# Kernel optimization log

Hardware: AMD Instinct MI355X
Metric: run time of the kernel (lower is better)

The kernel has to match this reference:

```python
import jax, jax.numpy as jnp
import numpy as np

B, K, N, D, E, EE, H, P = 512, 64, 1024, 128, 100000, 1024, 256, 12

def setup_inputs() -> dict:
    key = jax.random.key(0)
    ks = jax.random.split(key, 6)
    return {
        'ts_emb': jax.random.normal(ks[0], (B, D, N), jnp.float32),
        'event_table': jax.random.normal(ks[1], (E, EE), jnp.float32),
        'W_t': jax.random.normal(ks[2], (H, EE), jnp.float32) * 0.02,
        'b_t': jnp.zeros((H,), jnp.float32),
        'W_mm': jax.random.normal(ks[3], (P, H + D), jnp.float32) * 0.02,
        'b_mm': jnp.zeros((P,), jnp.float32),
        'W_ts': jax.random.normal(ks[4], (P, D), jnp.float32) * 0.02,
        'b_ts': jnp.zeros((P,), jnp.float32),
        'event_idx': jax.random.randint(ks[5], (B, K), 0, E, jnp.int64) if jax.config.read('jax_enable_x64') else jax.random.randint(ks[5], (B, K), 0, E, jnp.int32),
        'event_mask': jnp.ones((B, K), bool),
    }

def reference(ts_emb, event_table, W_t, b_t, W_mm, b_mm, W_ts, b_ts, event_idx, event_mask):
    h = W_t.shape[0]  # hidden_event_emb_dim
    # ragged event gather: [B, K, EE]
    ev = event_table[event_idx]
    # Linear(EE -> H): [B, K, H]
    ev_h = jnp.einsum('bke,he->bkh', ev, W_t) + b_t
    # masked max over events (event_fuse_type='max'): [B, H]
    neg = jnp.asarray(-jnp.inf, ev_h.dtype)
    ev_emb = jnp.max(jnp.where(event_mask[:, :, None], ev_h, neg), axis=1)
    # mm_forecaster = Conv1d(H+D -> P, k=1) on cat([event_emb repeat N, ts_emb]);
    # split the channel-wise linear so the broadcast part is never materialized.
    mm_ev = ev_emb @ W_mm[:, :h].T                       # [B, P]
    mm_ts = jnp.einsum('pd,bdn->bpn', W_mm[:, h:], ts_emb)  # [B, P, N]
    mm_pred = mm_ev[:, :, None] + mm_ts + b_mm[None, :, None]
    # ts_forecaster = Conv1d(D -> P, k=1)
    ts_pred = jnp.einsum('pd,bdn->bpn', W_ts, ts_emb) + b_ts[None, :, None]
    return (ts_pred + mm_pred) * 0.5
```

## Files before the change

### kernel.cpp

```cpp
#include <hip/hip_runtime.h>
#include <hip/hip_bf16.h>
#include <math.h>

#define B_   512
#define KEV  64
#define NN   1024
#define DD   128
#define EE_  1024
#define HH   256
#define PP   12
#define BKE  256
#define NSE  (EE_ / BKE)

typedef __bf16 bf16x8 __attribute__((ext_vector_type(8)));
typedef float  f32x4  __attribute__((ext_vector_type(4)));

static __device__ __forceinline__ unsigned short f2bf(float f) {
    unsigned int u = __builtin_bit_cast(unsigned int, f);
    u = (u + 0x7FFFu + ((u >> 16) & 1u)) >> 16;
    return (unsigned short)u;
}

__global__ __launch_bounds__(256) void prep_kernel(
    const float* __restrict__ Wt,
    const float* __restrict__ Wmm,
    const float* __restrict__ Wts,
    const unsigned int* __restrict__ idxW,
    const unsigned int* __restrict__ mskW,
    unsigned short* __restrict__ WtBf,
    float* __restrict__ Wc,
    int* __restrict__ flags)
{
    if (blockIdx.x < 256) {
        int i4 = (blockIdx.x * 256 + threadIdx.x) * 4;
        const float4 v = *reinterpret_cast<const float4*>(Wt + i4);
        ushort4 o = make_ushort4(f2bf(v.x), f2bf(v.y), f2bf(v.z), f2bf(v.w));
        *reinterpret_cast<ushort4*>(WtBf + i4) = o;
        return;
    }
    __shared__ int any_nz;
    if (threadIdx.x == 0) any_nz = 0;
    __syncthreads();
    int local = 0;
    for (int k = threadIdx.x; k < (B_ * KEV) / 2; k += 256)
        local |= (idxW[2 * k + 1] != 0u);
    if (local) atomicOr(&any_nz, 1);
    for (int k = threadIdx.x; k < PP * DD; k += 256) {
        int p = k >> 7, d = k & 127;
        Wc[k] = Wmm[p * (HH + DD) + HH + d] + Wts[p * DD + d];
    }
    __syncthreads();
    if (threadIdx.x == 0) {
        flags[0] = any_nz ? 0 : 1;
        unsigned int w0 = mskW[0], w1 = mskW[1];
        flags[1] = (w0 == 0x01010101u) ? 0 : ((w1 == 0u) ? 2 : 1);
    }
}

__global__ __launch_bounds__(256, 2) void event_kernel(
    const float* __restrict__ table,
    const void* __restrict__ idxRaw,
    const void* __restrict__ maskRaw,
    const int* __restrict__ flags,
    const unsigned short* __restrict__ WtBf,
    const float* __restrict__ bt,
    const float* __restrict__ Wmm,
    const float* __restrict__ bmm,
    const float* __restrict__ bts,
    float* __restrict__ cOut)
{
    const int b = blockIdx.x;
    const int t = threadIdx.x;
    const int w = t >> 6;
    const int l = t & 63;

    __shared__ __align__(16) unsigned short sA[2][64 * BKE];
    __shared__ int           sIdx[KEV];
    __shared__ unsigned char sMask[KEV];
    __shared__ float         sEv[HH];

    if (t < KEV) {
        const int i = b * KEV + t;
        int id;
        if (flags[0]) id = (int)((const long long*)idxRaw)[i];
        else          id = ((const int*)idxRaw)[i];
        sIdx[t] = id;
        const int mm = flags[1];
        bool mk;
        if      (mm == 0) mk = ((const unsigned char*)maskRaw)[i] != 0;
        else if (mm == 1) mk = ((const int*)maskRaw)[i] != 0;
        else              mk = ((const long long*)maskRaw)[i] != 0;
        sMask[t] = mk ? 1 : 0;
    }
    __syncthreads();

    const float* ptr[16];
    #pragma unroll
    for (int i = 0; i < 16; ++i)
        ptr[i] = table + (size_t)sIdx[w * 16 + i] * EE_ + (l << 2);

    auto loadstep = [&](int s, f32x4 (&r)[16]) {
        #pragma unroll
        for (int i = 0; i < 16; ++i)
            r[i] = *reinterpret_cast<const f32x4*>(ptr[i] + s * BKE);
    };
    auto writebuf = [&](int bufi, const f32x4 (&r)[16]) {
        #pragma unroll
        for (int i = 0; i < 16; ++i) {
            const int row = w * 16 + i;
            const int sw  = ((row & 7) << 3) ^ ((row & 8) << 1);
            ushort4 o = make_ushort4(f2bf(r[i][0]), f2bf(r[i][1]),
                                     f2bf(r[i][2]), f2bf(r[i][3]));
            *reinterpret_cast<ushort4*>(
                &sA[bufi][row * BKE + (((l << 2)) ^ sw)]) = o;
        }
    };

    const int lm = l & 15;
    const int lg = l >> 4;

    f32x4 acc[4][4];
    #pragma unroll
    for (int mi = 0; mi < 4; ++mi)
        #pragma unroll
        for (int ni = 0; ni < 4; ++ni)
            acc[mi][ni] = (f32x4){0.f, 0.f, 0.f, 0.f};

    const unsigned short* wtB = WtBf + (size_t)(w * 64 + lm) * EE_ + lg * 8;

    auto mfma_step = [&](int cur, int s) {
        #pragma unroll
        for (int ks = 0; ks < 8; ++ks) {
            bf16x8 af[4];
            #pragma unroll
            for (int mi = 0; mi < 4; ++mi) {
                const int row = mi * 16 + lm;
                const int e   = ks * 32 + lg * 8;
                const int es  = e ^ (((row & 7) << 3) ^ ((row & 8) << 1));
                af[mi] = *reinterpret_cast<const bf16x8*>(&sA[cur][row * BKE + es]);
            }
            #pragma unroll
            for (int ni = 0; ni < 4; ++ni) {
                const unsigned short* bp = wtB + (size_t)ni * 16 * EE_ + s * BKE + ks * 32;
                bf16x8 bfr = *reinterpret_cast<const bf16x8*>(bp);
                #pragma unroll
                for (int mi = 0; mi < 4; ++mi)
                    acc[mi][ni] = __builtin_amdgcn_mfma_f32_16x16x32_bf16(
                        af[mi], bfr, acc[mi][ni], 0, 0, 0);
            }
        }
    };

    f32x4 rA[16];
    loadstep(0, rA);
    writebuf(0, rA);
    __syncthreads();

    #pragma unroll 1
    for (int s = 0; s < NSE; ++s) {
        if (s + 1 < NSE) loadstep(s + 1, rA);
        mfma_step(s & 1, s);
        if (s + 1 < NSE) writebuf((s + 1) & 1, rA);
        __syncthreads();
    }

    #pragma unroll
    for (int ni = 0; ni < 4; ++ni) {
        float mx = -INFINITY;
        #pragma unroll
        for (int mi = 0; mi < 4; ++mi) {
            #pragma unroll
            for (int r = 0; r < 4; ++r) {
                const int ev = mi * 16 + lg * 4 + r;
                const float v = sMask[ev] ? acc[mi][ni][r] : -INFINITY;
                mx = fmaxf(mx, v);
            }
        }
        mx = fmaxf(mx, __shfl_xor(mx, 16));
        mx = fmaxf(mx, __shfl_xor(mx, 32));
        if (lg == 0) {
            const int h = w * 64 + ni * 16 + lm;
            sEv[h] = mx + bt[h];
        }
    }
    __syncthreads();

    if (w == 0) {
        #pragma unroll 1
        for (int p = 0; p < PP; ++p) {
            const float* wr = Wmm + p * (HH + DD);
            float sum = sEv[l]       * wr[l]
                      + sEv[l + 64]  * wr[l + 64]
                      + sEv[l + 128] * wr[l + 128]
                      + sEv[l + 192] * wr[l + 192];
            #pragma unroll
            for (int off = 32; off >= 1; off >>= 1) sum += __shfl_xor(sum, off);
            if (l == 0) cOut[b * PP + p] = sum + bmm[p] + bts[p];
        }
    }
}

__global__ __launch_bounds__(256) void ts_kernel(
    const float* __restrict__ ts,
    const float* __restrict__ Wc,
    const float* __restrict__ cIn,
    float* __restrict__ out)
{
    const int b = blockIdx.x;
    const int t = threadIdx.x;

    __shared__ float sC[PP];
    __shared__ float sWc[PP * DD];
    if (t < PP) sC[t] = cIn[b * PP + t];
    for (int k = t; k < (PP * DD) / 4; k += 256)
        reinterpret_cast<float4*>(sWc)[k] = reinterpret_cast<const float4*>(Wc)[k];
    __syncthreads();

    const float* tsb = ts + (size_t)b * DD * NN + t * 4;

    f32x4 acc[PP];
    #pragma unroll
    for (int p = 0; p < PP; ++p) {
        const float c = sC[p];
        acc[p] = (f32x4){c, c, c, c};
    }

    #pragma unroll 4
    for (int d = 0; d < DD; ++d) {
        const f32x4 v = __builtin_nontemporal_load(
            reinterpret_cast<const f32x4*>(tsb + (size_t)d * NN));
        #pragma unroll
        for (int p = 0; p < PP; ++p) {
            acc[p] += sWc[p * DD + d] * v;
        }
    }

    float* ob = out + (size_t)b * PP * NN + t * 4;
    #pragma unroll
    for (int p = 0; p < PP; ++p) {
        const f32x4 r = acc[p] * 0.5f;
        __builtin_nontemporal_store(r, reinterpret_cast<f32x4*>(ob + (size_t)p * NN));
    }
}

extern "C" void kernel_launch(void* const* d_in, const int* in_sizes, int n_in,
                              void* d_out, int out_size, void* d_ws, size_t ws_size,
                              hipStream_t stream)
{
    const float* ts    = (const float*)d_in[0];
    const float* table = (const float*)d_in[1];
    const float* Wt    = (const float*)d_in[2];
    const float* bt    = (const float*)d_in[3];
    const float* Wmm   = (const float*)d_in[4];
    const float* bmm   = (const float*)d_in[5];
    const float* Wts   = (const float*)d_in[6];
    const float* bts   = (const float*)d_in[7];
    const void*  idx   = (const void*)d_in[8];
    const void*  msk   = (const void*)d_in[9];
    float* out = (float*)d_out;

    unsigned short* WtBf = (unsigned short*)d_ws;
    float* Wc  = (float*)((char*)d_ws + (512u << 10));
    float* cB  = (float*)((char*)d_ws + (512u << 10) + 8192);
    int*   flg = (int*)((char*)d_ws + (512u << 10) + 8192 + B_ * PP * 4);

    prep_kernel<<<257, 256, 0, stream>>>(Wt, Wmm, Wts,
                                         (const unsigned int*)idx,
                                         (const unsigned int*)msk,
                                         WtBf, Wc, flg);
    event_kernel<<<B_, 256, 0, stream>>>(table, idx, msk, flg, WtBf, bt,
                                         Wmm, bmm, bts, cB);
    ts_kernel<<<B_, 256, 0, stream>>>(ts, Wc, cB, out);
}
```

Baseline: 115.6 us.

## Stage full gathered event tile in LDS and split ts kernel across two blocks

The event kernel now gathers all 64 event rows (full 1024 width) into one 128KB LDS tile up front, two rows at a time, then runs a single uninterrupted MFMA loop. This replaces the double-buffered 4-stage K pipeline and its per-stage barriers. sEv is aliased onto the LDS buffer and launch bounds drop to one block per CU, which gives up overlap between the gather and the MFMA work. The ts kernel uses two 128-thread blocks per batch row and batches 8 loads per iteration, with plain instead of nontemporal loads.

New measurement: 157.5 us. 36.3% more time.

```diff
diff --git a/kernel.cpp b/kernel.cpp
--- a/kernel.cpp
+++ b/kernel.cpp
@@ -9,11 +9,11 @@
 #define EE_  1024
 #define HH   256
 #define PP   12
-#define BKE  256
-#define NSE  (EE_ / BKE)
 
 typedef __bf16 bf16x8 __attribute__((ext_vector_type(8)));
 typedef float  f32x4  __attribute__((ext_vector_type(4)));
+
+#define SWZ(row) ((((row) & 7) << 3) ^ (((row) & 8) << 1))
 
 static __device__ __forceinline__ unsigned short f2bf(float f) {
     unsigned int u = __builtin_bit_cast(unsigned int, f);
@@ -57,7 +57,7 @@
     }
 }
 
-__global__ __launch_bounds__(256, 2) void event_kernel(
+__global__ __launch_bounds__(256, 1) void event_kernel(
     const float* __restrict__ table,
     const void* __restrict__ idxRaw,
     const void* __restrict__ maskRaw,
@@ -74,10 +74,10 @@
     const int w = t >> 6;
     const int l = t & 63;
 
-    __shared__ __align__(16) unsigned short sA[2][64 * BKE];
+    __shared__ __align__(16) unsigned short sA[64 * 1024];
     __shared__ int           sIdx[KEV];
     __shared__ unsigned char sMask[KEV];
-    __shared__ float         sEv[HH];
+    float* sEv = reinterpret_cast<float*>(sA);
 
     if (t < KEV) {
         const int i = b * KEV + t;
@@ -94,27 +94,35 @@
     }
     __syncthreads();
 
-    const float* ptr[16];
-    #pragma unroll
-    for (int i = 0; i < 16; ++i)
-        ptr[i] = table + (size_t)sIdx[w * 16 + i] * EE_ + (l << 2);
-
-    auto loadstep = [&](int s, f32x4 (&r)[16]) {
-        #pragma unroll
-        for (int i = 0; i < 16; ++i)
-            r[i] = *reinterpret_cast<const f32x4*>(ptr[i] + s * BKE);
+    const int r0 = w * 16;
+    f32x4 v0[4], v1[4];
+    auto loadrow = [&](int i, f32x4 (&v)[4]) {
+        const float* rp = table + (size_t)sIdx[r0 + i] * EE_ + (l << 2);
+        #pragma unroll
+        for (int c = 0; c < 4; ++c)
+            v[c] = *reinterpret_cast<const f32x4*>(rp + c * 256);
     };
-    auto writebuf = [&](int bufi, const f32x4 (&r)[16]) {
-        #pragma unroll
-        for (int i = 0; i < 16; ++i) {
-            const int row = w * 16 + i;
-            const int sw  = ((row & 7) << 3) ^ ((row & 8) << 1);
-            ushort4 o = make_ushort4(f2bf(r[i][0]), f2bf(r[i][1]),
-                                     f2bf(r[i][2]), f2bf(r[i][3]));
-            *reinterpret_cast<ushort4*>(
-                &sA[bufi][row * BKE + (((l << 2)) ^ sw)]) = o;
+    auto writerow = [&](int i, const f32x4 (&v)[4]) {
+        const int row = r0 + i;
+        unsigned short* base = sA + row * 1024;
+        const int sw = SWZ(row);
+        #pragma unroll
+        for (int c = 0; c < 4; ++c) {
+            ushort4 o = make_ushort4(f2bf(v[c][0]), f2bf(v[c][1]),
+                                     f2bf(v[c][2]), f2bf(v[c][3]));
+            *reinterpret_cast<ushort4*>(base + ((c * 256 + (l << 2)) ^ sw)) = o;
         }
     };
+
+    loadrow(0, v0);
+    #pragma unroll
+    for (int i = 0; i < 16; ++i) {
+        if (i + 1 < 16) {
+            if (i & 1) loadrow(i + 1, v0); else loadrow(i + 1, v1);
+        }
+        if (i & 1) writerow(i, v1); else writerow(i, v0);
+    }
+    __syncthreads();
 
     const int lm = l & 15;
     const int lg = l >> 4;
@@ -128,41 +136,26 @@
 
     const unsigned short* wtB = WtBf + (size_t)(w * 64 + lm) * EE_ + lg * 8;
 
-    auto mfma_step = [&](int cur, int s) {
-        #pragma unroll
-        for (int ks = 0; ks < 8; ++ks) {
-            bf16x8 af[4];
-            #pragma unroll
-            for (int mi = 0; mi < 4; ++mi) {
-                const int row = mi * 16 + lm;
-                const int e   = ks * 32 + lg * 8;
-                const int es  = e ^ (((row & 7) << 3) ^ ((row & 8) << 1));
-                af[mi] = *reinterpret_cast<const bf16x8*>(&sA[cur][row * BKE + es]);
-            }
-            #pragma unroll
-            for (int ni = 0; ni < 4; ++ni) {
-                const unsigned short* bp = wtB + (size_t)ni * 16 * EE_ + s * BKE + ks * 32;
-                bf16x8 bfr = *reinterpret_cast<const bf16x8*>(bp);
-                #pragma unroll
-                for (int mi = 0; mi < 4; ++mi)
-                    acc[mi][ni] = __builtin_amdgcn_mfma_f32_16x16x32_bf16(
-                        af[mi], bfr, acc[mi][ni], 0, 0, 0);
-            }
-        }
-    };
-
-    f32x4 rA[16];
-    loadstep(0, rA);
-    writebuf(0, rA);
-    __syncthreads();
-
-    #pragma unroll 1
-    for (int s = 0; s < NSE; ++s) {
-        if (s + 1 < NSE) loadstep(s + 1, rA);
-        mfma_step(s & 1, s);
-        if (s + 1 < NSE) writebuf((s + 1) & 1, rA);
-        __syncthreads();
-    }
+    #pragma unroll 4
+    for (int ks = 0; ks < 32; ++ks) {
+        bf16x8 af[4];
+        #pragma unroll
+        for (int mi = 0; mi < 4; ++mi) {
+            const int row = mi * 16 + lm;
+            const int e   = (ks * 32 + lg * 8) ^ SWZ(row);
+            af[mi] = *reinterpret_cast<const bf16x8*>(sA + row * 1024 + e);
+        }
+        #pragma unroll
+        for (int ni = 0; ni < 4; ++ni) {
+            bf16x8 bfr = *reinterpret_cast<const bf16x8*>(
+                wtB + (size_t)ni * 16 * EE_ + ks * 32);
+            #pragma unroll
+            for (int mi = 0; mi < 4; ++mi)
+                acc[mi][ni] = __builtin_amdgcn_mfma_f32_16x16x32_bf16(
+                    af[mi], bfr, acc[mi][ni], 0, 0, 0);
+        }
+    }
+    __syncthreads();
 
     #pragma unroll
     for (int ni = 0; ni < 4; ++ni) {
@@ -200,23 +193,24 @@
     }
 }
 
-__global__ __launch_bounds__(256) void ts_kernel(
+__global__ __launch_bounds__(128) void ts_kernel(
     const float* __restrict__ ts,
     const float* __restrict__ Wc,
     const float* __restrict__ cIn,
     float* __restrict__ out)
 {
-    const int b = blockIdx.x;
-    const int t = threadIdx.x;
+    const int t   = threadIdx.x;
+    const int b   = blockIdx.x >> 1;
+    const int half= blockIdx.x & 1;
 
     __shared__ float sC[PP];
     __shared__ float sWc[PP * DD];
     if (t < PP) sC[t] = cIn[b * PP + t];
-    for (int k = t; k < (PP * DD) / 4; k += 256)
+    for (int k = t; k < (PP * DD) / 4; k += 128)
         reinterpret_cast<float4*>(sWc)[k] = reinterpret_cast<const float4*>(Wc)[k];
     __syncthreads();
 
-    const float* tsb = ts + (size_t)b * DD * NN + t * 4;
+    const float* tsb = ts + (size_t)b * DD * NN + half * 512 + (t << 2);
 
     f32x4 acc[PP];
     #pragma unroll
@@ -225,17 +219,21 @@
         acc[p] = (f32x4){c, c, c, c};
     }
 
-    #pragma unroll 4
-    for (int d = 0; d < DD; ++d) {
-        const f32x4 v = __builtin_nontemporal_load(
-            reinterpret_cast<const f32x4*>(tsb + (size_t)d * NN));
-        #pragma unroll
-        for (int p = 0; p < PP; ++p) {
-            acc[p] += sWc[p * DD + d] * v;
-        }
-    }
-
-    float* ob = out + (size_t)b * PP * NN + t * 4;
+    #pragma unroll 1
+    for (int d0 = 0; d0 < DD; d0 += 8) {
+        f32x4 v[8];
+        #pragma unroll
+        for (int j = 0; j < 8; ++j)
+            v[j] = *reinterpret_cast<const f32x4*>(tsb + (size_t)(d0 + j) * NN);
+        #pragma unroll
+        for (int j = 0; j < 8; ++j) {
+            #pragma unroll
+            for (int p = 0; p < PP; ++p)
+                acc[p] += sWc[p * DD + d0 + j] * v[j];
+        }
+    }
+
+    float* ob = out + (size_t)b * PP * NN + half * 512 + (t << 2);
     #pragma unroll
     for (int p = 0; p < PP; ++p) {
         const f32x4 r = acc[p] * 0.5f;
@@ -270,5 +268,5 @@
                                          WtBf, Wc, flg);
     event_kernel<<<B_, 256, 0, stream>>>(table, idx, msk, flg, WtBf, bt,
                                          Wmm, bmm, bts, cB);
-    ts_kernel<<<B_, 256, 0, stream>>>(ts, Wc, cB, out);
-}
+    ts_kernel<<<2 * B_, 128, 0, stream>>>(ts, Wc, cB, out);
+}
```

## Load gathered event rows straight into MFMA registers and prefetch ts_emb

Applied to the files above, without the earlier changes.

The event kernel no longer stages gathered fp32 table rows into a double-buffered swizzled LDS tile. Each lane now loads its own 8 fp32 values per k-step directly from global memory and packs them to bf16 with v_cvt_pk_bf16_f32, which removes LDS traffic, the block-wide barriers and about 64KB of shared memory per block. In exchange, every wave re-reads the same A rows, so global and L2 traffic on the gather goes up roughly fourfold, and the loads are not hidden behind a separate staging step. The ts kernel swaps its unrolled nontemporal loop for an explicit two-buffer prefetch of 8 rows at a time, using plain loads instead of nontemporal ones.

Result: slower. 202.9 us (+75.6%).

```diff
diff --git a/kernel.cpp b/kernel.cpp
--- a/kernel.cpp
+++ b/kernel.cpp
@@ -9,8 +9,6 @@
 #define EE_  1024
 #define HH   256
 #define PP   12
-#define BKE  256
-#define NSE  (EE_ / BKE)
 
 typedef __bf16 bf16x8 __attribute__((ext_vector_type(8)));
 typedef float  f32x4  __attribute__((ext_vector_type(4)));
@@ -19,6 +17,17 @@
     unsigned int u = __builtin_bit_cast(unsigned int, f);
     u = (u + 0x7FFFu + ((u >> 16) & 1u)) >> 16;
     return (unsigned short)u;
+}
+
+static __device__ __forceinline__ bf16x8 cvt8(f32x4 lo, f32x4 hi) {
+    unsigned int r0, r1, r2, r3;
+    asm("v_cvt_pk_bf16_f32 %0, %1, %2" : "=v"(r0) : "v"(lo[0]), "v"(lo[1]));
+    asm("v_cvt_pk_bf16_f32 %0, %1, %2" : "=v"(r1) : "v"(lo[2]), "v"(lo[3]));
+    asm("v_cvt_pk_bf16_f32 %0, %1, %2" : "=v"(r2) : "v"(hi[0]), "v"(hi[1]));
+    asm("v_cvt_pk_bf16_f32 %0, %1, %2" : "=v"(r3) : "v"(hi[2]), "v"(hi[3]));
+    union { unsigned int u[4]; bf16x8 v; } o;
+    o.u[0] = r0; o.u[1] = r1; o.u[2] = r2; o.u[3] = r3;
+    return o.v;
 }
 
 __global__ __launch_bounds__(256) void prep_kernel(
@@ -73,8 +82,9 @@
     const int t = threadIdx.x;
     const int w = t >> 6;
     const int l = t & 63;
-
-    __shared__ __align__(16) unsigned short sA[2][64 * BKE];
+    const int lm = l & 15;
+    const int lg = l >> 4;
+
     __shared__ int           sIdx[KEV];
     __shared__ unsigned char sMask[KEV];
     __shared__ float         sEv[HH];
@@ -94,30 +104,12 @@
     }
     __syncthreads();
 
-    const float* ptr[16];
-    #pragma unroll
-    for (int i = 0; i < 16; ++i)
-        ptr[i] = table + (size_t)sIdx[w * 16 + i] * EE_ + (l << 2);
-
-    auto loadstep = [&](int s, f32x4 (&r)[16]) {
-        #pragma unroll
-        for (int i = 0; i < 16; ++i)
-            r[i] = *reinterpret_cast<const f32x4*>(ptr[i] + s * BKE);
-    };
-    auto writebuf = [&](int bufi, const f32x4 (&r)[16]) {
-        #pragma unroll
-        for (int i = 0; i < 16; ++i) {
-            const int row = w * 16 + i;
-            const int sw  = ((row & 7) << 3) ^ ((row & 8) << 1);
-            ushort4 o = make_ushort4(f2bf(r[i][0]), f2bf(r[i][1]),
-                                     f2bf(r[i][2]), f2bf(r[i][3]));
-            *reinterpret_cast<ushort4*>(
-                &sA[bufi][row * BKE + (((l << 2)) ^ sw)]) = o;
-        }
-    };
-
-    const int lm = l & 15;
-    const int lg = l >> 4;
+    const float* aptr[4];
+    #pragma unroll
+    for (int mi = 0; mi < 4; ++mi)
+        aptr[mi] = table + (size_t)sIdx[mi * 16 + lm] * EE_ + lg * 8;
+
+    const unsigned short* wtB = WtBf + (size_t)(w * 64 + lm) * EE_ + lg * 8;
 
     f32x4 acc[4][4];
     #pragma unroll
@@ -126,42 +118,24 @@
         for (int ni = 0; ni < 4; ++ni)
             acc[mi][ni] = (f32x4){0.f, 0.f, 0.f, 0.f};
 
-    const unsigned short* wtB = WtBf + (size_t)(w * 64 + lm) * EE_ + lg * 8;
-
-    auto mfma_step = [&](int cur, int s) {
-        #pragma unroll
-        for (int ks = 0; ks < 8; ++ks) {
-            bf16x8 af[4];
-            #pragma unroll
-            for (int mi = 0; mi < 4; ++mi) {
-                const int row = mi * 16 + lm;
-                const int e   = ks * 32 + lg * 8;
-                const int es  = e ^ (((row & 7) << 3) ^ ((row & 8) << 1));
-                af[mi] = *reinterpret_cast<const bf16x8*>(&sA[cur][row * BKE + es]);
-            }
-            #pragma unroll
-            for (int ni = 0; ni < 4; ++ni) {
-                const unsigned short* bp = wtB + (size_t)ni * 16 * EE_ + s * BKE + ks * 32;
-                bf16x8 bfr = *reinterpret_cast<const bf16x8*>(bp);
-                #pragma unroll
-                for (int mi = 0; mi < 4; ++mi)
-                    acc[mi][ni] = __builtin_amdgcn_mfma_f32_16x16x32_bf16(
-                        af[mi], bfr, acc[mi][ni], 0, 0, 0);
-            }
-        }
-    };
-
-    f32x4 rA[16];
-    loadstep(0, rA);
-    writebuf(0, rA);
-    __syncthreads();
-
-    #pragma unroll 1
-    for (int s = 0; s < NSE; ++s) {
-        if (s + 1 < NSE) loadstep(s + 1, rA);
-        mfma_step(s & 1, s);
-        if (s + 1 < NSE) writebuf((s + 1) & 1, rA);
-        __syncthreads();
+    #pragma unroll 2
+    for (int ks = 0; ks < 32; ++ks) {
+        bf16x8 af[4];
+        #pragma unroll
+        for (int mi = 0; mi < 4; ++mi) {
+            const f32x4 lo = *reinterpret_cast<const f32x4*>(aptr[mi] + ks * 32);
+            const f32x4 hi = *reinterpret_cast<const f32x4*>(aptr[mi] + ks * 32 + 4);
+            af[mi] = cvt8(lo, hi);
+        }
+        #pragma unroll
+        for (int ni = 0; ni < 4; ++ni) {
+            const bf16x8 bfr = *reinterpret_cast<const bf16x8*>(
+                wtB + (size_t)ni * 16 * EE_ + ks * 32);
+            #pragma unroll
+            for (int mi = 0; mi < 4; ++mi)
+                acc[mi][ni] = __builtin_amdgcn_mfma_f32_16x16x32_bf16(
+                    af[mi], bfr, acc[mi][ni], 0, 0, 0);
+        }
     }
 
     #pragma unroll
@@ -225,14 +199,29 @@
         acc[p] = (f32x4){c, c, c, c};
     }
 
-    #pragma unroll 4
-    for (int d = 0; d < DD; ++d) {
-        const f32x4 v = __builtin_nontemporal_load(
-            reinterpret_cast<const f32x4*>(tsb + (size_t)d * NN));
-        #pragma unroll
-        for (int p = 0; p < PP; ++p) {
-            acc[p] += sWc[p * DD + d] * v;
-        }
+    f32x4 vA[8], vB[8];
+
+    auto load8 = [&](f32x4 (&v)[8], int d0) {
+        #pragma unroll
+        for (int j = 0; j < 8; ++j)
+            v[j] = *reinterpret_cast<const f32x4*>(tsb + (size_t)(d0 + j) * NN);
+    };
+    auto fma8 = [&](const f32x4 (&v)[8], int d0) {
+        #pragma unroll
+        for (int j = 0; j < 8; ++j) {
+            #pragma unroll
+            for (int p = 0; p < PP; ++p)
+                acc[p] += sWc[p * DD + d0 + j] * v[j];
+        }
+    };
+
+    load8(vA, 0);
+    #pragma unroll 1
+    for (int d0 = 0; d0 < DD; d0 += 16) {
+        load8(vB, d0 + 8);
+        fma8(vA, d0);
+        if (d0 + 16 < DD) load8(vA, d0 + 16);
+        fma8(vB, d0 + 8);
     }
 
     float* ob = out + (size_t)b * PP * NN + t * 4;
```
